# Performance work log

Hardware: AMD Instinct MI355X
Metric: run time of the kernel (lower is better)

Reference implementation:

```python
import jax, jax.numpy as jnp
import numpy as np

B, S, D, U = 32, 2048, 512, 512

def setup_inputs() -> dict:
    key = jax.random.key(0)
    k1, k2, k3, k4, k5 = jax.random.split(key, 5)
    passage = jax.random.normal(k1, (B, S, D), dtype=jnp.float32)
    hidden = jax.random.normal(k2, (B, D), dtype=jnp.float32)
    mask = jnp.ones((B, S), dtype=jnp.float32)
    # learned params (Dense kernels, glorot-ish scale)
    W1 = jax.random.normal(k3, (D, U), dtype=jnp.float32) / np.sqrt(D)
    W2 = jax.random.normal(k4, (D, U), dtype=jnp.float32) / np.sqrt(D)
    Vw = jax.random.normal(k5, (U, 1), dtype=jnp.float32) / np.sqrt(U)
    Vb = jnp.zeros((1,), dtype=jnp.float32)
    return {"passage": passage, "hidden": hidden, "mask": mask,
            "W1": W1, "W2": W2, "Vw": Vw, "Vb": Vb}

def reference(passage, hidden, mask, W1, W2, Vw, Vb):
    # passage: [B,S,D], hidden: [B,D], mask: [B,S]
    h_proj = jnp.einsum('bd,du->bu', hidden, W2)[:, None, :]        # [B,1,U]
    p_proj = jnp.einsum('bsd,du->bsu', passage, W1)                  # [B,S,U]
    score = jnp.einsum('bsu,uo->bso', jnp.tanh(p_proj + h_proj), Vw) + Vb  # [B,S,1]
    score = score + ((1.0 - mask) * -1e30)[:, :, None]
    attention_weights = jax.nn.softmax(score, axis=1)                # [B,S,1]
    context_vector = jnp.sum(attention_weights * passage, axis=1)    # [B,D]
    return context_vector, attention_weights
```

## Files before the change

### kernel.cpp

```cpp
#include <hip/hip_runtime.h>
#include <hip/hip_bf16.h>
#include <cstddef>


#define NB 32
#define NS 2048
#define ND 512
#define NU 512

typedef __bf16 bf16_t;
typedef __bf16 bf16x8 __attribute__((ext_vector_type(8)));
typedef float floatx4 __attribute__((ext_vector_type(4)));

__device__ __forceinline__ void dma16(const void* g, void* l) {
    __builtin_amdgcn_global_load_lds(
        (const __attribute__((address_space(1))) unsigned int*)g,
        (__attribute__((address_space(3))) unsigned int*)l, 16, 0, 0);
}

__global__ __launch_bounds__(256) void prep_kernel(
    const float* __restrict__ W1, bf16_t* __restrict__ W1p,
    const float* __restrict__ hidden, const float* __restrict__ W2,
    float* __restrict__ hproj) {
    if (blockIdx.x < 128) {
        int wave = threadIdx.x >> 6, lane = threadIdx.x & 63;
        int f = (blockIdx.x << 2) + wave;
        int kc = f >> 5, ng = f & 31;
        int q = lane >> 4, c = lane & 15;
        const float* src = W1 + (kc * 32 + q * 8) * 512 + ng * 16 + c;
        bf16x8 w;
#pragma unroll
        for (int jj = 0; jj < 8; ++jj) w[jj] = (bf16_t)src[jj * 512];
        ((bf16x8*)W1p)[(f << 6) + lane] = w;
    } else {
        __shared__ float h[ND];
        __shared__ float part[256];
        int bi = blockIdx.x - 128;
        int b = bi >> 2, ug = bi & 3;
        int t = threadIdx.x;
        h[t] = hidden[b * ND + t];
        h[t + 256] = hidden[b * ND + t + 256];
        __syncthreads();
        int u = (ug << 7) + (t & 127);
        int d0 = (t >> 7) << 8;
        float acc = 0.f;
#pragma unroll 8
        for (int d = d0; d < d0 + 256; ++d) acc = fmaf(h[d], W2[d * NU + u], acc);
        part[t] = acc;
        __syncthreads();
        if (t < 128) hproj[b * NU + u] = part[t] + part[t + 128];
    }
}

__global__ __launch_bounds__(256, 3) void score_kernel(
    const float* __restrict__ passage, const bf16_t* __restrict__ W1p,
    const float* __restrict__ hproj, const float* __restrict__ Vw,
    const float* __restrict__ Vb, float* __restrict__ scores) {
    __shared__ float ring[2 * 64 * 32];
    __shared__ float red[4 * 64];
    const int tid = threadIdx.x;
    const int wave = tid >> 6, lane = tid & 63;
    const int q = lane >> 4, c = lane & 15;
    const int bid = blockIdx.x;
    const int mblk = ((bid >> 4) << 3) + (bid & 7);
    const int nhalf = (bid >> 3) & 1;
    const int m0 = mblk * 64;
    const int b = m0 >> 11;
    const int ng0 = (nhalf << 4) + (wave << 2);
    const bf16x8* Wq = (const bf16x8*)W1p;

    const int ch0 = wave * 2;
    const int r0 = ch0 * 8 + (lane >> 3);
    const int k0 = ((lane & 7) - r0) & 7;
    const int r1 = r0 + 8;
    const int k1 = ((lane & 7) - r1) & 7;
    const float* g0 = passage + (size_t)(m0 + r0) * ND + k0 * 4;
    const float* g1 = passage + (size_t)(m0 + r1) * ND + k1 * 4;
    char* l0a = (char*)ring + ch0 * 1024;
    char* l1a = (char*)ring + ch0 * 1024 + 1024;
    char* l0b = (char*)ring + 8192 + ch0 * 1024;
    char* l1b = (char*)ring + 8192 + ch0 * 1024 + 1024;

    dma16(g0, l0a);
    dma16(g1, l1a);
    __syncthreads();

    floatx4 acc[4][4];
#pragma unroll
    for (int i = 0; i < 4; ++i)
#pragma unroll
        for (int j = 0; j < 4; ++j) { floatx4 z = {0.f, 0.f, 0.f, 0.f}; acc[i][j] = z; }

    for (int kc = 0; kc < 16; ++kc) {
        if (kc < 15) {
            const float* ga = g0 + (kc + 1) * 32;
            const float* gb = g1 + (kc + 1) * 32;
            if ((kc + 1) & 1) { dma16(ga, l0b); dma16(gb, l1b); }
            else              { dma16(ga, l0a); dma16(gb, l1a); }
        }
        bf16x8 bb[4];
#pragma unroll
        for (int j = 0; j < 4; ++j)
            bb[j] = Wq[(((kc << 5) + ng0 + j) << 6) + lane];
        const float* sl = ring + (kc & 1) * 2048;
#pragma unroll
        for (int i = 0; i < 4; ++i) {
            int r = i * 16 + c;
            const float* rp = sl + r * 32;
            floatx4 lo = *(const floatx4*)(rp + (((q << 1) + r) & 7) * 4);
            floatx4 hi = *(const floatx4*)(rp + (((q << 1) + 1 + r) & 7) * 4);
            bf16x8 a;
            a[0] = (bf16_t)lo[0]; a[1] = (bf16_t)lo[1];
            a[2] = (bf16_t)lo[2]; a[3] = (bf16_t)lo[3];
            a[4] = (bf16_t)hi[0]; a[5] = (bf16_t)hi[1];
            a[6] = (bf16_t)hi[2]; a[7] = (bf16_t)hi[3];
#pragma unroll
            for (int j = 0; j < 4; ++j)
                acc[i][j] = __builtin_amdgcn_mfma_f32_16x16x32_bf16(a, bb[j], acc[i][j], 0, 0, 0);
        }
        __syncthreads();
    }

    float sp[4][4];
#pragma unroll
    for (int i = 0; i < 4; ++i)
#pragma unroll
        for (int r = 0; r < 4; ++r) sp[i][r] = 0.f;
#pragma unroll
    for (int j = 0; j < 4; ++j) {
        int n = ((ng0 + j) << 4) + c;
        float hp = hproj[(b << 9) + n];
        float vw = Vw[n];
#pragma unroll
        for (int i = 0; i < 4; ++i)
#pragma unroll
            for (int r = 0; r < 4; ++r) {
                float x = acc[i][j][r] + hp;
                float e = __expf(2.0f * x);
                float t = 1.0f - 2.0f * __builtin_amdgcn_rcpf(e + 1.0f);
                sp[i][r] = fmaf(t, vw, sp[i][r]);
            }
    }
#pragma unroll
    for (int off = 1; off < 16; off <<= 1)
#pragma unroll
        for (int i = 0; i < 4; ++i)
#pragma unroll
            for (int r = 0; r < 4; ++r)
                sp[i][r] += __shfl_xor(sp[i][r], off, 64);

    if (c == 0) {
#pragma unroll
        for (int i = 0; i < 4; ++i)
#pragma unroll
            for (int r = 0; r < 4; ++r)
                red[(wave << 6) + i * 16 + q * 4 + r] = sp[i][r];
    }
    __syncthreads();
    if (tid < 64) {
        float s = red[tid] + red[64 + tid] + red[128 + tid] + red[192 + tid];
        if (nhalf == 0) s += Vb[0];
        atomicAdd(&scores[m0 + tid], s);
    }
}

__global__ __launch_bounds__(1024) void softmax_kernel(
    const float* __restrict__ mask, float* __restrict__ attn) {
    __shared__ float smx[16], ssm[16];
    int b = blockIdx.x, tid = threadIdx.x;
    int wave = tid >> 6, lane = tid & 63;
    const int base = b * NS;
    float v0 = attn[base + tid] + (1.0f - mask[base + tid]) * (-1e30f);
    float v1 = attn[base + 1024 + tid] + (1.0f - mask[base + 1024 + tid]) * (-1e30f);
    float mx = fmaxf(v0, v1);
#pragma unroll
    for (int off = 1; off < 64; off <<= 1) mx = fmaxf(mx, __shfl_xor(mx, off, 64));
    if (lane == 0) smx[wave] = mx;
    __syncthreads();
    mx = smx[0];
#pragma unroll
    for (int w = 1; w < 16; ++w) mx = fmaxf(mx, smx[w]);
    v0 = __expf(v0 - mx); v1 = __expf(v1 - mx);
    float sum = v0 + v1;
#pragma unroll
    for (int off = 1; off < 64; off <<= 1) sum += __shfl_xor(sum, off, 64);
    if (lane == 0) ssm[wave] = sum;
    __syncthreads();
    sum = 0.f;
#pragma unroll
    for (int w = 0; w < 16; ++w) sum += ssm[w];
    float inv = 1.0f / sum;
    attn[base + tid] = v0 * inv;
    attn[base + 1024 + tid] = v1 * inv;
}

__global__ __launch_bounds__(512) void context_kernel(
    const float* __restrict__ passage, const float* __restrict__ attn,
    float* __restrict__ ctx) {
    __shared__ float4 part[512];
    int bb = blockIdx.x >> 5, sc = blockIdx.x & 31, t = threadIdx.x;
    int col = t & 127, qh = t >> 7;
    const float4* p = (const float4*)(passage + (((size_t)bb * NS + sc * 64 + qh * 16) << 9));
    const float* wp = attn + bb * NS + sc * 64 + qh * 16;
    float ax = 0.f, ay = 0.f, az = 0.f, aw = 0.f;
#pragma unroll 16
    for (int s = 0; s < 16; ++s) {
        float w = wp[s];
        float4 v = p[(size_t)s * 128 + col];
        ax = fmaf(w, v.x, ax); ay = fmaf(w, v.y, ay);
        az = fmaf(w, v.z, az); aw = fmaf(w, v.w, aw);
    }
    float4 mine; mine.x = ax; mine.y = ay; mine.z = az; mine.w = aw;
    part[t] = mine;
    __syncthreads();
    if (t < 128) {
        float4 o1 = part[t + 128], o2 = part[t + 256], o3 = part[t + 384];
        float* dst = ctx + bb * ND + t * 4;
        atomicAdd(dst + 0, ax + o1.x + o2.x + o3.x);
        atomicAdd(dst + 1, ay + o1.y + o2.y + o3.y);
        atomicAdd(dst + 2, az + o1.z + o2.z + o3.z);
        atomicAdd(dst + 3, aw + o1.w + o2.w + o3.w);
    }
}

extern "C" void kernel_launch(void* const* d_in, const int* in_sizes, int n_in,
                              void* d_out, int out_size, void* d_ws, size_t ws_size,
                              hipStream_t stream) {
    const float* passage = (const float*)d_in[0];
    const float* hidden  = (const float*)d_in[1];
    const float* mask    = (const float*)d_in[2];
    const float* W1      = (const float*)d_in[3];
    const float* W2      = (const float*)d_in[4];
    const float* Vw      = (const float*)d_in[5];
    const float* Vb      = (const float*)d_in[6];

    float* ctx  = (float*)d_out;
    float* attn = (float*)d_out + NB * ND;

    bf16_t* W1p  = (bf16_t*)d_ws;
    float* hproj = (float*)((char*)d_ws + (size_t)NU * ND * 2);

    hipMemsetAsync(ctx, 0, (size_t)NB * (ND + NS) * sizeof(float), stream);
    prep_kernel<<<dim3(256), dim3(256), 0, stream>>>(W1, W1p, hidden, W2, hproj);
    score_kernel<<<dim3(2 * NB * NS / 64), dim3(256), 0, stream>>>(passage, W1p, hproj, Vw, Vb, attn);
    softmax_kernel<<<dim3(NB), dim3(1024), 0, stream>>>(mask, attn);
    context_kernel<<<dim3(NB * 32), dim3(512), 0, stream>>>(passage, attn, ctx);
}
```

Measured before the change: 278.3 us.

## Deepen passage DMA ring to four slots and double-buffer W1 fragments

Expands the LDS staging ring from two to four slices so three passage slices are in flight, and prefetches next-iteration W1 bf16 fragments into a register double buffer. Replaces the per-iteration __syncthreads with a partial vmcnt wait plus s_barrier so outstanding loads are not drained each step. This aims to hide global load latency in the memory-bound score GEMM, at the cost of doubled LDS use and a hand-counted vmcnt that depends on exact load ordering.

Measured after the change: 270.5 us. -2.8%, faster.

```diff
diff --git a/kernel.cpp b/kernel.cpp
--- a/kernel.cpp
+++ b/kernel.cpp
@@ -56,7 +56,7 @@
     const float* __restrict__ passage, const bf16_t* __restrict__ W1p,
     const float* __restrict__ hproj, const float* __restrict__ Vw,
     const float* __restrict__ Vb, float* __restrict__ scores) {
-    __shared__ float ring[2 * 64 * 32];
+    __shared__ float ring[4 * 64 * 32];
     __shared__ float red[4 * 64];
     const int tid = threadIdx.x;
     const int wave = tid >> 6, lane = tid & 63;
@@ -76,14 +76,23 @@
     const int k1 = ((lane & 7) - r1) & 7;
     const float* g0 = passage + (size_t)(m0 + r0) * ND + k0 * 4;
     const float* g1 = passage + (size_t)(m0 + r1) * ND + k1 * 4;
-    char* l0a = (char*)ring + ch0 * 1024;
-    char* l1a = (char*)ring + ch0 * 1024 + 1024;
-    char* l0b = (char*)ring + 8192 + ch0 * 1024;
-    char* l1b = (char*)ring + 8192 + ch0 * 1024 + 1024;
-
-    dma16(g0, l0a);
-    dma16(g1, l1a);
-    __syncthreads();
+
+#define DMA_SLICE(slice) do {                                         \
+        char* _l = (char*)ring + ((slice) & 3) * 8192 + ch0 * 1024;   \
+        dma16(g0 + (slice) * 32, _l);                                 \
+        dma16(g1 + (slice) * 32, _l + 1024);                          \
+    } while (0)
+
+    DMA_SLICE(0);
+    DMA_SLICE(1);
+    DMA_SLICE(2);
+    asm volatile("" ::: "memory");
+    bf16x8 bb[2][4];
+#pragma unroll
+    for (int j = 0; j < 4; ++j)
+        bb[0][j] = Wq[((ng0 + j) << 6) + lane];
+    asm volatile("s_waitcnt vmcnt(8)" ::: "memory");
+    __builtin_amdgcn_s_barrier();
 
     floatx4 acc[4][4];
 #pragma unroll
@@ -91,18 +100,16 @@
 #pragma unroll
         for (int j = 0; j < 4; ++j) { floatx4 z = {0.f, 0.f, 0.f, 0.f}; acc[i][j] = z; }
 
+#pragma unroll
     for (int kc = 0; kc < 16; ++kc) {
         if (kc < 15) {
-            const float* ga = g0 + (kc + 1) * 32;
-            const float* gb = g1 + (kc + 1) * 32;
-            if ((kc + 1) & 1) { dma16(ga, l0b); dma16(gb, l1b); }
-            else              { dma16(ga, l0a); dma16(gb, l1a); }
+#pragma unroll
+            for (int j = 0; j < 4; ++j)
+                bb[(kc + 1) & 1][j] = Wq[((((kc + 1) << 5) + ng0 + j) << 6) + lane];
         }
-        bf16x8 bb[4];
-#pragma unroll
-        for (int j = 0; j < 4; ++j)
-            bb[j] = Wq[(((kc << 5) + ng0 + j) << 6) + lane];
-        const float* sl = ring + (kc & 1) * 2048;
+        if (kc + 3 < 16) DMA_SLICE(kc + 3);
+
+        const float* sl = ring + (kc & 3) * 2048;
 #pragma unroll
         for (int i = 0; i < 4; ++i) {
             int r = i * 16 + c;
@@ -116,10 +123,14 @@
             a[6] = (bf16_t)hi[2]; a[7] = (bf16_t)hi[3];
 #pragma unroll
             for (int j = 0; j < 4; ++j)
-                acc[i][j] = __builtin_amdgcn_mfma_f32_16x16x32_bf16(a, bb[j], acc[i][j], 0, 0, 0);
+                acc[i][j] = __builtin_amdgcn_mfma_f32_16x16x32_bf16(a, bb[kc & 1][j], acc[i][j], 0, 0, 0);
         }
-        __syncthreads();
-    }
+        if (kc < 15) {
+            asm volatile("s_waitcnt vmcnt(8)" ::: "memory");
+            __builtin_amdgcn_s_barrier();
+        }
+    }
+#undef DMA_SLICE
 
     float sp[4][4];
 #pragma unroll
```
